# Kernel tuning notes

Measured on AMD Instinct MI355X. Metric: run time of the kernel, lower is better.

The kernel has to match this reference:

```python
import jax, jax.numpy as jnp
import numpy as np

N, E, H, HEADS = 50000, 800000, 64, 4
EPS = 1e-5
NEG_SLOPE = 0.2


def _ln(x, g, b):
    mu = x.mean(-1, keepdims=True)
    var = x.var(-1, keepdims=True)
    return (x - mu) / jnp.sqrt(var + EPS) * g + b


def _gat(x, row, col, W, a_src, a_dst, bias, heads, out_dim, concat):
    # PyG GATConv: add self-loops, linear, per-edge attention, segment softmax, scatter-agg
    n = x.shape[0]
    loop = jnp.arange(n, dtype=row.dtype)
    r = jnp.concatenate([row, loop])  # message sources
    c = jnp.concatenate([col, loop])  # message targets (aggregation index)
    h = (x @ W).reshape(n, heads, out_dim)              # [N, heads, out]
    a_s = jnp.sum(h * a_src, axis=-1)                   # [N, heads]
    a_d = jnp.sum(h * a_dst, axis=-1)                   # [N, heads]
    e = jax.nn.leaky_relu(a_s[r] + a_d[c], NEG_SLOPE)   # [E', heads]
    m = jax.ops.segment_max(e, c, num_segments=n)       # stable softmax per target node
    p = jnp.exp(e - m[c])
    alpha = p / jax.ops.segment_sum(p, c, num_segments=n)[c]
    out = jax.ops.segment_sum(h[r] * alpha[..., None], c, num_segments=n)  # [N, heads, out]
    out = out.reshape(n, heads * out_dim) if concat else out.mean(axis=1)
    return out + bias


def setup_inputs() -> dict:
    key = jax.random.key(0)
    ks = jax.random.split(key, 16)
    d = {}
    d["node_embeds"] = jax.random.normal(ks[0], (N, H), jnp.float32)
    d["edge_index"] = jax.random.randint(ks[1], (2, E), 0, N, jnp.int32)
    d["edge_embeds"] = jax.random.normal(ks[2], (E, H), jnp.float32)
    layer_cfg = [(H, HEADS, H, True), (H * HEADS, HEADS, H, True), (H * HEADS, 1, H, False)]
    i = 3
    for li, (din, heads, dout, concat) in enumerate(layer_cfg):
        d[f"W{li}"] = jax.random.normal(ks[i], (din, heads * dout), jnp.float32) * 0.05; i += 1
        d[f"asrc{li}"] = jax.random.normal(ks[i], (heads, dout), jnp.float32) * 0.05; i += 1
        d[f"adst{li}"] = jax.random.normal(ks[i], (heads, dout), jnp.float32) * 0.05; i += 1
        odim = heads * dout if concat else dout
        d[f"b{li}"] = jnp.zeros((odim,), jnp.float32)
        d[f"g{li}"] = jnp.ones((odim,), jnp.float32)
        d[f"be{li}"] = jnp.zeros((odim,), jnp.float32)
    return d


def reference(node_embeds, edge_index, edge_embeds,
              W0, asrc0, adst0, b0, g0, be0,
              W1, asrc1, adst1, b1, g1, be1,
              W2, asrc2, adst2, b2, g2, be2):
    row, col = edge_index[0], edge_index[1]
    # scatter-mean edge embeddings onto target nodes (reduce='mean', clamp count>=1)
    cnt = jnp.maximum(jax.ops.segment_sum(jnp.ones((E,), jnp.float32), col, num_segments=N), 1.0)
    x = node_embeds + jax.ops.segment_sum(edge_embeds, col, num_segments=N) / cnt[:, None]
    layers = [
        (W0, asrc0, adst0, b0, g0, be0, HEADS, True),
        (W1, asrc1, adst1, b1, g1, be1, HEADS, True),
        (W2, asrc2, adst2, b2, g2, be2, 1, False),
    ]
    for (W, a_s, a_d, b, g, be, heads, concat) in layers:
        x = _gat(x, row, col, W, a_s, a_d, b, heads, H, concat)
        x = jax.nn.elu(_ln(x, g, be))
        # dropout: identity in eval mode
    return x
```

## Files before the change

kernel.cpp:

```cpp
#include <hip/hip_runtime.h>
#include <math.h>

#define NN 50000
#define NE 800000
#define MPAD 50048

typedef __attribute__((ext_vector_type(8))) short bf16x8;
typedef __attribute__((ext_vector_type(8))) unsigned short u16x8;
typedef __attribute__((ext_vector_type(4))) float f32x4;

__device__ __forceinline__ float leaky(float x){ return x > 0.f ? x : 0.2f*x; }

__device__ __forceinline__ unsigned short f2bf(float f){
  unsigned int u = __float_as_uint(f);
  unsigned int r = (u + 0x7fffu + ((u >> 16) & 1u)) >> 16;
  return (unsigned short)r;
}
__device__ __forceinline__ float bf2f(unsigned short u){
  return __uint_as_float(((unsigned int)u) << 16);
}

__global__ void k_zero(int* __restrict__ deg){
  int i = blockIdx.x*blockDim.x + threadIdx.x;
  if (i < NN) deg[i] = 0;
}

__global__ void k_hist(const int* __restrict__ col, int* __restrict__ deg){
  int e = blockIdx.x*blockDim.x + threadIdx.x;
  if (e < NE) atomicAdd(&deg[col[e]], 1);
}

__global__ void k_scan(const int* __restrict__ deg, int* __restrict__ off, int* __restrict__ cursor){
  __shared__ int buf[1024];
  __shared__ int carry_s;
  if (threadIdx.x==0) carry_s = 0;
  __syncthreads();
  for (int base=0; base<NN; base+=1024){
    int i = base + (int)threadIdx.x;
    int v = (i<NN)? deg[i] : 0;
    buf[threadIdx.x] = v;
    __syncthreads();
    for (int s=1;s<1024;s<<=1){
      int t = (threadIdx.x >= (unsigned)s)? buf[threadIdx.x-s] : 0;
      __syncthreads();
      buf[threadIdx.x] += t;
      __syncthreads();
    }
    int excl = carry_s + buf[threadIdx.x] - v;
    if (i<NN){ off[i]=excl; cursor[i]=excl; }
    __syncthreads();
    if (threadIdx.x==1023) carry_s += buf[1023];
    __syncthreads();
  }
  if (threadIdx.x==0) off[NN]=carry_s;
}

__global__ void k_scatter(const int* __restrict__ row, const int* __restrict__ col,
                          int* __restrict__ cursor, int* __restrict__ esrc, int* __restrict__ eid){
  int e = blockIdx.x*blockDim.x + threadIdx.x;
  if (e < NE){
    int c = col[e];
    int pos = atomicAdd(&cursor[c], 1);
    esrc[pos] = row[e];
    eid[pos]  = e;
  }
}

__global__ void k_premix(const float* __restrict__ node, const float* __restrict__ ee,
                         const int* __restrict__ off, const int* __restrict__ eid,
                         unsigned short* __restrict__ Xb){
  int wid  = (int)((blockIdx.x*blockDim.x + threadIdx.x) >> 6);
  int lane = threadIdx.x & 63;
  if (wid >= NN) return;
  int g   = lane >> 4;
  int l16 = lane & 15;
  int s0 = off[wid], s1 = off[wid+1];

  float a0=0.f, a1=0.f, a2=0.f, a3=0.f;
  for (int p = s0 + g; p < s1; p += 4){
    int ed = eid[p];
    float4 hv = *reinterpret_cast<const float4*>(ee + (size_t)ed*64 + l16*4);
    a0 += hv.x; a1 += hv.y; a2 += hv.z; a3 += hv.w;
  }
  #pragma unroll
  for (int mk=16; mk<64; mk<<=1){
    a0 += __shfl_xor(a0, mk, 64);
    a1 += __shfl_xor(a1, mk, 64);
    a2 += __shfl_xor(a2, mk, 64);
    a3 += __shfl_xor(a3, mk, 64);
  }
  if (lane < 16){
    int dcnt = s1 - s0;
    float c = (float)(dcnt > 1 ? dcnt : 1);
    float4 nv = *reinterpret_cast<const float4*>(node + (size_t)wid*64 + l16*4);
    ushort4 o;
    o.x = f2bf(nv.x + a0 / c);
    o.y = f2bf(nv.y + a1 / c);
    o.z = f2bf(nv.z + a2 / c);
    o.w = f2bf(nv.w + a3 / c);
    *reinterpret_cast<ushort4*>(Xb + (size_t)wid*64 + l16*4) = o;
  }
}

__global__ void k_wconv(const float* __restrict__ W, unsigned short* __restrict__ Wt,
                        int K, int Ncols){
  int idx = blockIdx.x*blockDim.x + threadIdx.x;
  if (idx < K*Ncols){
    int n = idx / K, k = idx - n*K;
    Wt[idx] = f2bf(W[(size_t)k*Ncols + n]);
  }
}

template<int BN, int K>
__global__ __launch_bounds__(256)
void k_gemm_mfma(const unsigned short* __restrict__ A,
                 const unsigned short* __restrict__ Bt,
                 unsigned short* __restrict__ C, int Nc){
  constexpr int BM = 128, BK = 32;
  constexpr int WNT = BN/32;
  __shared__ __align__(16) unsigned short As[BM*BK];
  __shared__ __align__(16) unsigned short Bs[BN*BK];
  const int tid  = threadIdx.x;
  const int lane = tid & 63;
  const int wid  = tid >> 6;
  const int wr   = wid >> 1, wc = wid & 1;
  const int bm   = blockIdx.y * BM, bn = blockIdx.x * BN;
  const int r    = lane >> 2, kq = lane & 3;

  f32x4 acc[4][WNT];
  #pragma unroll
  for (int i=0;i<4;++i)
    #pragma unroll
    for (int j=0;j<WNT;++j) acc[i][j] = (f32x4){0.f,0.f,0.f,0.f};

  for (int k0=0; k0<K; k0+=BK){
    #pragma unroll
    for (int i=0;i<2;++i){
      int arow = wid*32 + i*16 + r;
      __builtin_amdgcn_global_load_lds(
        (const __attribute__((address_space(1))) void*)(A + (size_t)(bm+arow)*K + k0 + kq*8),
        (__attribute__((address_space(3))) void*)&As[(wid*32 + i*16)*BK],
        16, 0, 0);
    }
    #pragma unroll
    for (int i=0;i<BN/64;++i){
      int brow = wid*(BN/4) + i*16 + r;
      __builtin_amdgcn_global_load_lds(
        (const __attribute__((address_space(1))) void*)(Bt + (size_t)(bn+brow)*K + k0 + kq*8),
        (__attribute__((address_space(3))) void*)&Bs[(wid*(BN/4) + i*16)*BK],
        16, 0, 0);
    }
    __syncthreads();

    bf16x8 af[4], bfr[WNT];
    #pragma unroll
    for (int mi=0; mi<4; ++mi)
      af[mi] = *reinterpret_cast<const bf16x8*>(&As[(wr*64 + mi*16 + (lane&15))*BK + (lane>>4)*8]);
    #pragma unroll
    for (int ni=0; ni<WNT; ++ni)
      bfr[ni] = *reinterpret_cast<const bf16x8*>(&Bs[(wc*(BN/2) + ni*16 + (lane&15))*BK + (lane>>4)*8]);
    #pragma unroll
    for (int mi=0; mi<4; ++mi)
      #pragma unroll
      for (int ni=0; ni<WNT; ++ni)
        acc[mi][ni] = __builtin_amdgcn_mfma_f32_16x16x32_bf16(af[mi], bfr[ni], acc[mi][ni], 0, 0, 0);
    __syncthreads();
  }

  #pragma unroll
  for (int mi=0; mi<4; ++mi){
    #pragma unroll
    for (int ni=0; ni<WNT; ++ni){
      int ccol = bn + wc*(BN/2) + ni*16 + (lane&15);
      int rbase = bm + wr*64 + mi*16 + (lane>>4)*4;
      #pragma unroll
      for (int reg=0; reg<4; ++reg)
        C[(size_t)(rbase+reg)*Nc + ccol] = f2bf(acc[mi][ni][reg]);
    }
  }
}

template<int HEADS>
__global__ void k_coef(const unsigned short* __restrict__ Hb, const float* __restrict__ asrc,
                       const float* __restrict__ adst,
                       float* __restrict__ AS, float* __restrict__ AD){
  constexpr int D   = HEADS*64;
  constexpr int VPL = D/64;
  constexpr int G   = 64/HEADS;
  int wid  = (int)((blockIdx.x*blockDim.x + threadIdx.x) >> 6);
  int lane = threadIdx.x & 63;
  if (wid >= NN) return;
  float s_=0.f, d_=0.f;
  if constexpr (VPL==4){
    ushort4 hv = *reinterpret_cast<const ushort4*>(Hb + (size_t)wid*D + lane*4);
    unsigned short hs[4] = {hv.x, hv.y, hv.z, hv.w};
    #pragma unroll
    for (int v=0; v<4; ++v){
      int idx = lane*4 + v;
      float h = bf2f(hs[v]);
      s_ += h * asrc[idx];
      d_ += h * adst[idx];
    }
  } else {
    float h = bf2f(Hb[(size_t)wid*D + lane]);
    s_ = h * asrc[lane];
    d_ = h * adst[lane];
  }
  #pragma unroll
  for (int mk=1; mk<G; mk<<=1){
    s_ += __shfl_xor(s_, mk, 64);
    d_ += __shfl_xor(d_, mk, 64);
  }
  if ((lane & (G-1)) == 0){
    int head = lane / G;
    AS[(size_t)wid*HEADS + head] = s_;
    AD[(size_t)wid*HEADS + head] = d_;
  }
}

template<int HEADS, bool OUT_BF16>
__global__ void k_agg(const unsigned short* __restrict__ Hb, const float* __restrict__ AS,
                      const float* __restrict__ AD, const int* __restrict__ off,
                      const int* __restrict__ esrc,
                      const float* __restrict__ bias, const float* __restrict__ gamma,
                      const float* __restrict__ beta, void* __restrict__ OutP){
  constexpr int D  = HEADS*64;
  constexpr int L  = (HEADS==4) ? 32 : 16;
  constexpr int C  = D / L;
  constexpr int NG = 64 / L;
  int wid  = (int)((blockIdx.x*blockDim.x + threadIdx.x) >> 6);
  int lane = threadIdx.x & 63;
  if (wid >= NN) return;
  const int g    = lane / L;
  const int lrow = lane & (L-1);
  const int col0 = lrow * C;
  const int head = col0 >> 6;

  float ad    = AD[(size_t)wid*HEADS + head];
  float wself = leaky(AS[(size_t)wid*HEADS + head] + ad);
  int s0 = off[wid], s1 = off[wid+1];

  float m, psum;
  float acc[C];
  if (g == 0){
    m = wself; psum = 1.f;
    if constexpr (C==8){
      u16x8 hv = *reinterpret_cast<const u16x8*>(Hb + (size_t)wid*D + col0);
      #pragma unroll
      for (int v=0;v<8;++v) acc[v] = bf2f((unsigned short)hv[v]);
    } else {
      ushort4 hv = *reinterpret_cast<const ushort4*>(Hb + (size_t)wid*D + col0);
      acc[0]=bf2f(hv.x); acc[1]=bf2f(hv.y); acc[2]=bf2f(hv.z); acc[3]=bf2f(hv.w);
    }
  } else {
    m = -1e30f; psum = 0.f;
    #pragma unroll
    for (int v=0;v<C;++v) acc[v]=0.f;
  }

  for (int p = s0 + g; p < s1; p += NG){
    int src = esrc[p];
    float w = leaky(AS[(size_t)src*HEADS + head] + ad);
    float mn = fmaxf(m, w);
    float scale = __expf(m - mn);
    float pw    = __expf(w - mn);
    m = mn;
    psum = psum*scale + pw;
    if constexpr (C==8){
      u16x8 hv = *reinterpret_cast<const u16x8*>(Hb + (size_t)src*D + col0);
      #pragma unroll
      for (int v=0;v<8;++v) acc[v] = acc[v]*scale + pw*bf2f((unsigned short)hv[v]);
    } else {
      ushort4 hv = *reinterpret_cast<const ushort4*>(Hb + (size_t)src*D + col0);
      acc[0] = acc[0]*scale + pw*bf2f(hv.x);
      acc[1] = acc[1]*scale + pw*bf2f(hv.y);
      acc[2] = acc[2]*scale + pw*bf2f(hv.z);
      acc[3] = acc[3]*scale + pw*bf2f(hv.w);
    }
  }

  #pragma unroll
  for (int mk=L; mk<64; mk<<=1){
    float m_o    = __shfl_xor(m, mk, 64);
    float psum_o = __shfl_xor(psum, mk, 64);
    float mn = fmaxf(m, m_o);
    float sA = __expf(m - mn);
    float sB = __expf(m_o - mn);
    psum = psum*sA + psum_o*sB;
    #pragma unroll
    for (int v=0;v<C;++v){
      float a_o = __shfl_xor(acc[v], mk, 64);
      acc[v] = acc[v]*sA + a_o*sB;
    }
    m = mn;
  }

  float inv = 1.f/psum;
  float val[C];
  float s=0.f, s2=0.f;
  #pragma unroll
  for (int v=0;v<C;++v){
    val[v] = acc[v]*inv + bias[col0+v];
    s  += val[v];
    s2 += val[v]*val[v];
  }
  #pragma unroll
  for (int mk=1; mk<64; mk<<=1){
    s  += __shfl_xor(s,  mk, 64);
    s2 += __shfl_xor(s2, mk, 64);
  }
  float mean = s/(float)(64*C);
  float var  = s2/(float)(64*C) - mean*mean;
  float rstd = rsqrtf(var + 1e-5f);
  if (g == 0){
    if constexpr (OUT_BF16){
      u16x8 o;
      #pragma unroll
      for (int v=0;v<C;++v){
        float y = (val[v]-mean)*rstd*gamma[col0+v] + beta[col0+v];
        y = (y > 0.f) ? y : expm1f(y);
        o[v] = f2bf(y);
      }
      if constexpr (C==8){
        *reinterpret_cast<u16x8*>((unsigned short*)OutP + (size_t)wid*D + col0) = o;
      } else {
        ushort4 o4; o4.x=(unsigned short)o[0]; o4.y=(unsigned short)o[1];
        o4.z=(unsigned short)o[2]; o4.w=(unsigned short)o[3];
        *reinterpret_cast<ushort4*>((unsigned short*)OutP + (size_t)wid*D + col0) = o4;
      }
    } else {
      float o[C];
      #pragma unroll
      for (int v=0;v<C;++v){
        float y = (val[v]-mean)*rstd*gamma[col0+v] + beta[col0+v];
        o[v] = (y > 0.f) ? y : expm1f(y);
      }
      if constexpr (C==4){
        float4 o4 = {o[0],o[1],o[2],o[3]};
        *reinterpret_cast<float4*>((float*)OutP + (size_t)wid*D + col0) = o4;
      } else {
        #pragma unroll
        for (int v=0;v<C;++v) ((float*)OutP)[(size_t)wid*D + col0+v] = o[v];
      }
    }
  }
}

extern "C" void kernel_launch(void* const* d_in, const int* in_sizes, int n_in,
                              void* d_out, int out_size, void* d_ws, size_t ws_size,
                              hipStream_t stream) {
  const float* node  = (const float*)d_in[0];
  const int*   eidx  = (const int*)d_in[1];
  const float* ee    = (const float*)d_in[2];
  const float* W0    = (const float*)d_in[3];
  const float* asrc0 = (const float*)d_in[4];
  const float* adst0 = (const float*)d_in[5];
  const float* b0    = (const float*)d_in[6];
  const float* g0    = (const float*)d_in[7];
  const float* be0   = (const float*)d_in[8];
  const float* W1    = (const float*)d_in[9];
  const float* asrc1 = (const float*)d_in[10];
  const float* adst1 = (const float*)d_in[11];
  const float* b1    = (const float*)d_in[12];
  const float* g1    = (const float*)d_in[13];
  const float* be1   = (const float*)d_in[14];
  const float* W2    = (const float*)d_in[15];
  const float* asrc2 = (const float*)d_in[16];
  const float* adst2 = (const float*)d_in[17];
  const float* b2    = (const float*)d_in[18];
  const float* g2    = (const float*)d_in[19];
  const float* be2   = (const float*)d_in[20];

  const int* row = eidx;
  const int* col = eidx + NE;

  unsigned short* Hb  = (unsigned short*)d_ws;
  unsigned short* Xb0 = Hb  + (size_t)MPAD*256;
  unsigned short* Xb  = Xb0 + (size_t)MPAD*64;
  unsigned short* Wt0 = Xb  + (size_t)MPAD*256;
  unsigned short* Wt1 = Wt0 + 256*64;
  unsigned short* Wt2 = Wt1 + 256*256;
  float* AS  = (float*)(Wt2 + 64*256);
  float* AD  = AS + (size_t)NN*4;
  int* deg   = (int*)(AD + (size_t)NN*4);
  int* off   = deg + NN;
  int* cursor= off + NN + 1;
  int* esrc  = cursor + NN;
  int* eid   = esrc + NE;

  float* out = (float*)d_out;

  k_zero<<<(NN+255)/256, 256, 0, stream>>>(deg);
  k_hist<<<(NE+255)/256, 256, 0, stream>>>(col, deg);
  k_scan<<<1, 1024, 0, stream>>>(deg, off, cursor);
  k_scatter<<<(NE+255)/256, 256, 0, stream>>>(row, col, cursor, esrc, eid);

  k_wconv<<<(256*64 +255)/256, 256, 0, stream>>>(W0, Wt0, 64, 256);
  k_wconv<<<(256*256+255)/256, 256, 0, stream>>>(W1, Wt1, 256, 256);
  k_wconv<<<(64*256 +255)/256, 256, 0, stream>>>(W2, Wt2, 256, 64);

  int nwaveblk = (NN*64 + 255)/256;
  k_premix<<<nwaveblk, 256, 0, stream>>>(node, ee, off, eid, Xb0);

  {
    dim3 g(256/128, MPAD/128);
    k_gemm_mfma<128,64><<<g, 256, 0, stream>>>(Xb0, Wt0, Hb, 256);
    k_coef<4><<<nwaveblk, 256, 0, stream>>>(Hb, asrc0, adst0, AS, AD);
    k_agg<4,true><<<nwaveblk, 256, 0, stream>>>(Hb, AS, AD, off, esrc, b0, g0, be0, Xb);
  }
  {
    dim3 g(256/128, MPAD/128);
    k_gemm_mfma<128,256><<<g, 256, 0, stream>>>(Xb, Wt1, Hb, 256);
    k_coef<4><<<nwaveblk, 256, 0, stream>>>(Hb, asrc1, adst1, AS, AD);
    k_agg<4,true><<<nwaveblk, 256, 0, stream>>>(Hb, AS, AD, off, esrc, b1, g1, be1, Xb);
  }
  {
    dim3 g(64/64, MPAD/128);
    k_gemm_mfma<64,256><<<g, 256, 0, stream>>>(Xb, Wt2, Hb, 64);
    k_coef<1><<<nwaveblk, 256, 0, stream>>>(Hb, asrc2, adst2, AS, AD);
    k_agg<1,false><<<nwaveblk, 256, 0, stream>>>(Hb, AS, AD, off, esrc, b2, g2, be2, out);
  }
}
```

Baseline: 536.7 us.

## Fuse attention coefficients into GEMM epilogue, parallelize scan, widen per-lane vectors

Drops the separate per-layer attention-coefficient kernels. The GEMM epilogue now computes the source and destination dot products from the fp32 accumulators and adds them into zeroed per-layer buffers with atomics. The single-block serial scan becomes a three-kernel multi-block scan. The premix and aggregation kernels now give each lane eight contiguous elements via 16-byte loads, using fewer lanes per row. The trade-offs are extra float atomics in the GEMM, a slightly different summation order from the atomics, and a larger zeroing kernel.

```diff
diff --git a/kernel.cpp b/kernel.cpp
--- a/kernel.cpp
+++ b/kernel.cpp
@@ -4,6 +4,7 @@
 #define NN 50000
 #define NE 800000
 #define MPAD 50048
+#define NB 196
 
 typedef __attribute__((ext_vector_type(8))) short bf16x8;
 typedef __attribute__((ext_vector_type(8))) unsigned short u16x8;
@@ -20,9 +21,17 @@
   return __uint_as_float(((unsigned int)u) << 16);
 }
 
-__global__ void k_zero(int* __restrict__ deg){
+__global__ void k_zero(int* __restrict__ deg,
+                       float* __restrict__ AS0, float* __restrict__ AD0,
+                       float* __restrict__ AS1, float* __restrict__ AD1,
+                       float* __restrict__ AS2, float* __restrict__ AD2){
   int i = blockIdx.x*blockDim.x + threadIdx.x;
   if (i < NN) deg[i] = 0;
+  if (i < NN*4){
+    AS0[i]=0.f; AD0[i]=0.f;
+    AS1[i]=0.f; AD1[i]=0.f;
+    AS2[i]=0.f; AD2[i]=0.f;
+  }
 }
 
 __global__ void k_hist(const int* __restrict__ col, int* __restrict__ deg){
@@ -30,29 +39,58 @@
   if (e < NE) atomicAdd(&deg[col[e]], 1);
 }
 
-__global__ void k_scan(const int* __restrict__ deg, int* __restrict__ off, int* __restrict__ cursor){
-  __shared__ int buf[1024];
-  __shared__ int carry_s;
-  if (threadIdx.x==0) carry_s = 0;
+__global__ void k_scan1(const int* __restrict__ deg, int* __restrict__ off,
+                        int* __restrict__ bsum){
+  __shared__ int ws[4];
+  int t = threadIdx.x;
+  int i = blockIdx.x*256 + t;
+  int v = (i<NN)? deg[i] : 0;
+  int lane = t & 63, w = t >> 6;
+  int x = v;
+  #pragma unroll
+  for (int d=1; d<64; d<<=1){
+    int y = __shfl_up(x, d, 64);
+    if (lane >= d) x += y;
+  }
+  if (lane==63) ws[w] = x;
   __syncthreads();
-  for (int base=0; base<NN; base+=1024){
-    int i = base + (int)threadIdx.x;
-    int v = (i<NN)? deg[i] : 0;
-    buf[threadIdx.x] = v;
-    __syncthreads();
-    for (int s=1;s<1024;s<<=1){
-      int t = (threadIdx.x >= (unsigned)s)? buf[threadIdx.x-s] : 0;
-      __syncthreads();
-      buf[threadIdx.x] += t;
-      __syncthreads();
-    }
-    int excl = carry_s + buf[threadIdx.x] - v;
-    if (i<NN){ off[i]=excl; cursor[i]=excl; }
-    __syncthreads();
-    if (threadIdx.x==1023) carry_s += buf[1023];
-    __syncthreads();
-  }
-  if (threadIdx.x==0) off[NN]=carry_s;
+  int woff = 0;
+  #pragma unroll
+  for (int k=0;k<3;++k) if (k < w) woff += ws[k];
+  int incl = x + woff;
+  if (i<NN) off[i] = incl - v;
+  if (t==255) bsum[blockIdx.x] = incl;
+}
+
+__global__ void k_scan2(int* __restrict__ bsum, int* __restrict__ off){
+  __shared__ int ws[4];
+  int t = threadIdx.x;
+  int v = (t<NB)? bsum[t] : 0;
+  int lane = t & 63, w = t >> 6;
+  int x = v;
+  #pragma unroll
+  for (int d=1; d<64; d<<=1){
+    int y = __shfl_up(x, d, 64);
+    if (lane >= d) x += y;
+  }
+  if (lane==63) ws[w] = x;
+  __syncthreads();
+  int woff = 0;
+  #pragma unroll
+  for (int k=0;k<3;++k) if (k < w) woff += ws[k];
+  int incl = x + woff;
+  if (t<NB) bsum[t] = incl - v;
+  if (t==NB-1) off[NN] = incl;
+}
+
+__global__ void k_scan3(const int* __restrict__ bsum, int* __restrict__ off,
+                        int* __restrict__ cursor){
+  int i = blockIdx.x*256 + threadIdx.x;
+  if (i<NN){
+    int v = off[i] + bsum[blockIdx.x];
+    off[i] = v;
+    cursor[i] = v;
+  }
 }
 
 __global__ void k_scatter(const int* __restrict__ row, const int* __restrict__ col,
@@ -72,33 +110,35 @@
   int wid  = (int)((blockIdx.x*blockDim.x + threadIdx.x) >> 6);
   int lane = threadIdx.x & 63;
   if (wid >= NN) return;
-  int g   = lane >> 4;
-  int l16 = lane & 15;
+  int g  = lane >> 3;
+  int l8 = lane & 7;
   int s0 = off[wid], s1 = off[wid+1];
 
-  float a0=0.f, a1=0.f, a2=0.f, a3=0.f;
-  for (int p = s0 + g; p < s1; p += 4){
+  float a[8];
+  #pragma unroll
+  for (int v=0;v<8;++v) a[v]=0.f;
+  for (int p = s0 + g; p < s1; p += 8){
     int ed = eid[p];
-    float4 hv = *reinterpret_cast<const float4*>(ee + (size_t)ed*64 + l16*4);
-    a0 += hv.x; a1 += hv.y; a2 += hv.z; a3 += hv.w;
-  }
-  #pragma unroll
-  for (int mk=16; mk<64; mk<<=1){
-    a0 += __shfl_xor(a0, mk, 64);
-    a1 += __shfl_xor(a1, mk, 64);
-    a2 += __shfl_xor(a2, mk, 64);
-    a3 += __shfl_xor(a3, mk, 64);
-  }
-  if (lane < 16){
+    const float4* rp = reinterpret_cast<const float4*>(ee + (size_t)ed*64 + l8*8);
+    float4 h0 = rp[0], h1 = rp[1];
+    a[0]+=h0.x; a[1]+=h0.y; a[2]+=h0.z; a[3]+=h0.w;
+    a[4]+=h1.x; a[5]+=h1.y; a[6]+=h1.z; a[7]+=h1.w;
+  }
+  #pragma unroll
+  for (int mk=8; mk<64; mk<<=1){
+    #pragma unroll
+    for (int v=0;v<8;++v) a[v] += __shfl_xor(a[v], mk, 64);
+  }
+  if (lane < 8){
     int dcnt = s1 - s0;
-    float c = (float)(dcnt > 1 ? dcnt : 1);
-    float4 nv = *reinterpret_cast<const float4*>(node + (size_t)wid*64 + l16*4);
-    ushort4 o;
-    o.x = f2bf(nv.x + a0 / c);
-    o.y = f2bf(nv.y + a1 / c);
-    o.z = f2bf(nv.z + a2 / c);
-    o.w = f2bf(nv.w + a3 / c);
-    *reinterpret_cast<ushort4*>(Xb + (size_t)wid*64 + l16*4) = o;
+    float c = 1.f/(float)(dcnt > 1 ? dcnt : 1);
+    const float4* np = reinterpret_cast<const float4*>(node + (size_t)wid*64 + l8*8);
+    float4 n0 = np[0], n1 = np[1];
+    float nv[8] = {n0.x,n0.y,n0.z,n0.w,n1.x,n1.y,n1.z,n1.w};
+    u16x8 o;
+    #pragma unroll
+    for (int v=0;v<8;++v) o[v] = f2bf(nv[v] + a[v]*c);
+    *reinterpret_cast<u16x8*>(Xb + (size_t)wid*64 + l8*8) = o;
   }
 }
 
@@ -111,11 +151,13 @@
   }
 }
 
-template<int BN, int K>
+template<int BN, int K, int HEADS>
 __global__ __launch_bounds__(256)
 void k_gemm_mfma(const unsigned short* __restrict__ A,
                  const unsigned short* __restrict__ Bt,
-                 unsigned short* __restrict__ C, int Nc){
+                 unsigned short* __restrict__ C,
+                 const float* __restrict__ asrc, const float* __restrict__ adst,
+                 float* __restrict__ AS, float* __restrict__ AD, int Nc){
   constexpr int BM = 128, BK = 32;
   constexpr int WNT = BN/32;
   __shared__ __align__(16) unsigned short As[BM*BK];
@@ -167,6 +209,15 @@
     __syncthreads();
   }
 
+  const int head = (bn + wc*(BN/2)) >> 6;
+  float av[WNT], dv[WNT];
+  #pragma unroll
+  for (int ni=0; ni<WNT; ++ni){
+    int ccol = bn + wc*(BN/2) + ni*16 + (lane&15);
+    av[ni] = asrc[ccol];
+    dv[ni] = adst[ccol];
+  }
+
   #pragma unroll
   for (int mi=0; mi<4; ++mi){
     #pragma unroll
@@ -177,44 +228,29 @@
       for (int reg=0; reg<4; ++reg)
         C[(size_t)(rbase+reg)*Nc + ccol] = f2bf(acc[mi][ni][reg]);
     }
-  }
-}
-
-template<int HEADS>
-__global__ void k_coef(const unsigned short* __restrict__ Hb, const float* __restrict__ asrc,
-                       const float* __restrict__ adst,
-                       float* __restrict__ AS, float* __restrict__ AD){
-  constexpr int D   = HEADS*64;
-  constexpr int VPL = D/64;
-  constexpr int G   = 64/HEADS;
-  int wid  = (int)((blockIdx.x*blockDim.x + threadIdx.x) >> 6);
-  int lane = threadIdx.x & 63;
-  if (wid >= NN) return;
-  float s_=0.f, d_=0.f;
-  if constexpr (VPL==4){
-    ushort4 hv = *reinterpret_cast<const ushort4*>(Hb + (size_t)wid*D + lane*4);
-    unsigned short hs[4] = {hv.x, hv.y, hv.z, hv.w};
-    #pragma unroll
-    for (int v=0; v<4; ++v){
-      int idx = lane*4 + v;
-      float h = bf2f(hs[v]);
-      s_ += h * asrc[idx];
-      d_ += h * adst[idx];
-    }
-  } else {
-    float h = bf2f(Hb[(size_t)wid*D + lane]);
-    s_ = h * asrc[lane];
-    d_ = h * adst[lane];
-  }
-  #pragma unroll
-  for (int mk=1; mk<G; mk<<=1){
-    s_ += __shfl_xor(s_, mk, 64);
-    d_ += __shfl_xor(d_, mk, 64);
-  }
-  if ((lane & (G-1)) == 0){
-    int head = lane / G;
-    AS[(size_t)wid*HEADS + head] = s_;
-    AD[(size_t)wid*HEADS + head] = d_;
+    float sp[4] = {0.f,0.f,0.f,0.f}, dp[4] = {0.f,0.f,0.f,0.f};
+    #pragma unroll
+    for (int ni=0; ni<WNT; ++ni)
+      #pragma unroll
+      for (int reg=0; reg<4; ++reg){
+        sp[reg] += acc[mi][ni][reg]*av[ni];
+        dp[reg] += acc[mi][ni][reg]*dv[ni];
+      }
+    #pragma unroll
+    for (int reg=0; reg<4; ++reg)
+      #pragma unroll
+      for (int mk=1; mk<16; mk<<=1){
+        sp[reg] += __shfl_xor(sp[reg], mk, 64);
+        dp[reg] += __shfl_xor(dp[reg], mk, 64);
+      }
+    if ((lane & 15) == 0){
+      int rr = bm + wr*64 + mi*16 + (lane>>4)*4;
+      #pragma unroll
+      for (int reg=0; reg<4; ++reg){
+        atomicAdd(&AS[(size_t)(rr+reg)*HEADS + head], sp[reg]);
+        atomicAdd(&AD[(size_t)(rr+reg)*HEADS + head], dp[reg]);
+      }
+    }
   }
 }
 
@@ -225,9 +261,10 @@
                       const float* __restrict__ bias, const float* __restrict__ gamma,
                       const float* __restrict__ beta, void* __restrict__ OutP){
   constexpr int D  = HEADS*64;
-  constexpr int L  = (HEADS==4) ? 32 : 16;
+  constexpr int L  = (HEADS==4) ? 16 : 8;
   constexpr int C  = D / L;
   constexpr int NG = 64 / L;
+  constexpr int NV = C / 8;
   int wid  = (int)((blockIdx.x*blockDim.x + threadIdx.x) >> 6);
   int lane = threadIdx.x & 63;
   if (wid >= NN) return;
@@ -244,14 +281,12 @@
   float acc[C];
   if (g == 0){
     m = wself; psum = 1.f;
-    if constexpr (C==8){
-      u16x8 hv = *reinterpret_cast<const u16x8*>(Hb + (size_t)wid*D + col0);
-      #pragma unroll
-      for (int v=0;v<8;++v) acc[v] = bf2f((unsigned short)hv[v]);
-    } else {
-      ushort4 hv = *reinterpret_cast<const ushort4*>(Hb + (size_t)wid*D + col0);
-      acc[0]=bf2f(hv.x); acc[1]=bf2f(hv.y); acc[2]=bf2f(hv.z); acc[3]=bf2f(hv.w);
-    }
+    const u16x8* hp = reinterpret_cast<const u16x8*>(Hb + (size_t)wid*D + col0);
+    u16x8 hv[NV];
+    #pragma unroll
+    for (int q=0;q<NV;++q) hv[q] = hp[q];
+    #pragma unroll
+    for (int v=0;v<C;++v) acc[v] = bf2f((unsigned short)hv[v>>3][v&7]);
   } else {
     m = -1e30f; psum = 0.f;
     #pragma unroll
@@ -266,17 +301,12 @@
     float pw    = __expf(w - mn);
     m = mn;
     psum = psum*scale + pw;
-    if constexpr (C==8){
-      u16x8 hv = *reinterpret_cast<const u16x8*>(Hb + (size_t)src*D + col0);
-      #pragma unroll
-      for (int v=0;v<8;++v) acc[v] = acc[v]*scale + pw*bf2f((unsigned short)hv[v]);
-    } else {
-      ushort4 hv = *reinterpret_cast<const ushort4*>(Hb + (size_t)src*D + col0);
-      acc[0] = acc[0]*scale + pw*bf2f(hv.x);
-      acc[1] = acc[1]*scale + pw*bf2f(hv.y);
-      acc[2] = acc[2]*scale + pw*bf2f(hv.z);
-      acc[3] = acc[3]*scale + pw*bf2f(hv.w);
-    }
+    const u16x8* hp = reinterpret_cast<const u16x8*>(Hb + (size_t)src*D + col0);
+    u16x8 hv[NV];
+    #pragma unroll
+    for (int q=0;q<NV;++q) hv[q] = hp[q];
+    #pragma unroll
+    for (int v=0;v<C;++v) acc[v] = acc[v]*scale + pw*bf2f((unsigned short)hv[v>>3][v&7]);
   }
 
   #pragma unroll
@@ -314,20 +344,16 @@
   float rstd = rsqrtf(var + 1e-5f);
   if (g == 0){
     if constexpr (OUT_BF16){
-      u16x8 o;
+      u16x8 o[NV];
       #pragma unroll
       for (int v=0;v<C;++v){
         float y = (val[v]-mean)*rstd*gamma[col0+v] + beta[col0+v];
         y = (y > 0.f) ? y : expm1f(y);
-        o[v] = f2bf(y);
-      }
-      if constexpr (C==8){
-        *reinterpret_cast<u16x8*>((unsigned short*)OutP + (size_t)wid*D + col0) = o;
-      } else {
-        ushort4 o4; o4.x=(unsigned short)o[0]; o4.y=(unsigned short)o[1];
-        o4.z=(unsigned short)o[2]; o4.w=(unsigned short)o[3];
-        *reinterpret_cast<ushort4*>((unsigned short*)OutP + (size_t)wid*D + col0) = o4;
-      }
+        o[v>>3][v&7] = f2bf(y);
+      }
+      u16x8* op = reinterpret_cast<u16x8*>((unsigned short*)OutP + (size_t)wid*D + col0);
+      #pragma unroll
+      for (int q=0;q<NV;++q) op[q] = o[q];
     } else {
       float o[C];
       #pragma unroll
@@ -335,12 +361,11 @@
         float y = (val[v]-mean)*rstd*gamma[col0+v] + beta[col0+v];
         o[v] = (y > 0.f) ? y : expm1f(y);
       }
-      if constexpr (C==4){
-        float4 o4 = {o[0],o[1],o[2],o[3]};
-        *reinterpret_cast<float4*>((float*)OutP + (size_t)wid*D + col0) = o4;
-      } else {
-        #pragma unroll
-        for (int v=0;v<C;++v) ((float*)OutP)[(size_t)wid*D + col0+v] = o[v];
+      float4* op = reinterpret_cast<float4*>((float*)OutP + (size_t)wid*D + col0);
+      #pragma unroll
+      for (int q=0;q<C/4;++q){
+        float4 o4 = {o[q*4+0],o[q*4+1],o[q*4+2],o[q*4+3]};
+        op[q] = o4;
       }
     }
   }
@@ -380,19 +405,26 @@
   unsigned short* Wt0 = Xb  + (size_t)MPAD*256;
   unsigned short* Wt1 = Wt0 + 256*64;
   unsigned short* Wt2 = Wt1 + 256*256;
-  float* AS  = (float*)(Wt2 + 64*256);
-  float* AD  = AS + (size_t)NN*4;
-  int* deg   = (int*)(AD + (size_t)NN*4);
+  float* AS0 = (float*)(Wt2 + 64*256);
+  float* AD0 = AS0 + (size_t)MPAD*4;
+  float* AS1 = AD0 + (size_t)MPAD*4;
+  float* AD1 = AS1 + (size_t)MPAD*4;
+  float* AS2 = AD1 + (size_t)MPAD*4;
+  float* AD2 = AS2 + (size_t)MPAD*4;
+  int* deg   = (int*)(AD2 + (size_t)MPAD*4);
   int* off   = deg + NN;
   int* cursor= off + NN + 1;
   int* esrc  = cursor + NN;
   int* eid   = esrc + NE;
+  int* bsum  = eid + NE;
 
   float* out = (float*)d_out;
 
-  k_zero<<<(NN+255)/256, 256, 0, stream>>>(deg);
+  k_zero<<<(NN*4+255)/256, 256, 0, stream>>>(deg, AS0, AD0, AS1, AD1, AS2, AD2);
   k_hist<<<(NE+255)/256, 256, 0, stream>>>(col, deg);
-  k_scan<<<1, 1024, 0, stream>>>(deg, off, cursor);
+  k_scan1<<<NB, 256, 0, stream>>>(deg, off, bsum);
+  k_scan2<<<1, 256, 0, stream>>>(bsum, off);
+  k_scan3<<<NB, 256, 0, stream>>>(bsum, off, cursor);
   k_scatter<<<(NE+255)/256, 256, 0, stream>>>(row, col, cursor, esrc, eid);
 
   k_wconv<<<(256*64 +255)/256, 256, 0, stream>>>(W0, Wt0, 64, 256);
@@ -404,20 +436,17 @@
 
   {
     dim3 g(256/128, MPAD/128);
-    k_gemm_mfma<128,64><<<g, 256, 0, stream>>>(Xb0, Wt0, Hb, 256);
-    k_coef<4><<<nwaveblk, 256, 0, stream>>>(Hb, asrc0, adst0, AS, AD);
-    k_agg<4,true><<<nwaveblk, 256, 0, stream>>>(Hb, AS, AD, off, esrc, b0, g0, be0, Xb);
+    k_gemm_mfma<128,64,4><<<g, 256, 0, stream>>>(Xb0, Wt0, Hb, asrc0, adst0, AS0, AD0, 256);
+    k_agg<4,true><<<nwaveblk, 256, 0, stream>>>(Hb, AS0, AD0, off, esrc, b0, g0, be0, Xb);
   }
   {
     dim3 g(256/128, MPAD/128);
-    k_gemm_mfma<128,256><<<g, 256, 0, stream>>>(Xb, Wt1, Hb, 256);
-    k_coef<4><<<nwaveblk, 256, 0, stream>>>(Hb, asrc1, adst1, AS, AD);
-    k_agg<4,true><<<nwaveblk, 256, 0, stream>>>(Hb, AS, AD, off, esrc, b1, g1, be1, Xb);
+    k_gemm_mfma<128,256,4><<<g, 256, 0, stream>>>(Xb, Wt1, Hb, asrc1, adst1, AS1, AD1, 256);
+    k_agg<4,true><<<nwaveblk, 256, 0, stream>>>(Hb, AS1, AD1, off, esrc, b1, g1, be1, Xb);
   }
   {
     dim3 g(64/64, MPAD/128);
-    k_gemm_mfma<64,256><<<g, 256, 0, stream>>>(Xb, Wt2, Hb, 64);
-    k_coef<1><<<nwaveblk, 256, 0, stream>>>(Hb, asrc2, adst2, AS, AD);
-    k_agg<1,false><<<nwaveblk, 256, 0, stream>>>(Hb, AS, AD, off, esrc, b2, g2, be2, out);
-  }
-}
+    k_gemm_mfma<64,256,1><<<g, 256, 0, stream>>>(Xb, Wt2, Hb, asrc2, adst2, AS2, AD2, 64);
+    k_agg<1,false><<<nwaveblk, 256, 0, stream>>>(Hb, AS2, AD2, off, esrc, b2, g2, be2, out);
+  }
+}
```

New measurement: 497.3 us. 7.3% less time.
